# Kernel tuning notes

Hardware: AMD Instinct MI355X
Metric: run time of the kernel (lower is better)

## Reference

```python
import jax, jax.numpy as jnp
import numpy as np

SEQ, B, I, H = 512, 64, 1024, 1024

def setup_inputs() -> dict:
    key = jax.random.key(0)
    ks = jax.random.split(key, 6)
    scale_ih = 1.0 / np.sqrt(I)
    scale_hh = 1.0 / np.sqrt(H)
    return {
        "input": jax.random.normal(ks[0], (SEQ, B, I), dtype=jnp.float32),
        "h_0": jax.random.normal(ks[1], (1, B, H), dtype=jnp.float32),
        "weight_ih": jax.random.normal(ks[2], (3 * H, I), dtype=jnp.float32) * scale_ih,
        "weight_hh": jax.random.normal(ks[3], (3 * H, H), dtype=jnp.float32) * scale_hh,
        "bias_ih": jax.random.normal(ks[4], (3 * H,), dtype=jnp.float32) * scale_hh,
        "bias_hh": jax.random.normal(ks[5], (3 * H,), dtype=jnp.float32) * scale_hh,
    }


def _gru_lbr0(input, h0, weight_ih, weight_hh, bias_ih, bias_hh):
    """Unidirectional GRU, ONNX linear_before_reset=0 semantics.

    r_t = sigmoid(x W_ir^T + b_ir + h W_hr^T + b_hr)
    z_t = sigmoid(x W_iz^T + b_iz + h W_hz^T + b_hz)
    n_t = tanh(x W_in^T + b_in + (r_t * h) W_hn^T + b_hn)
    h_t = (1 - z_t) * n_t + z_t * h
    """
    hidden = h0.shape[-1]
    # Precompute all input projections in one big GEMM: (S, B, 3H)
    gx = jnp.einsum('sbi,gi->sbg', input, weight_ih) + bias_ih
    W_hr, W_hz, W_hn = jnp.split(weight_hh, 3, axis=0)
    b_hr, b_hz, b_hn = jnp.split(bias_hh, 3, axis=0)

    def step(h, gx_t):
        gx_r, gx_z, gx_n = jnp.split(gx_t, 3, axis=-1)
        r = jax.nn.sigmoid(gx_r + h @ W_hr.T + b_hr)
        z = jax.nn.sigmoid(gx_z + h @ W_hz.T + b_hz)
        n = jnp.tanh(gx_n + (r * h) @ W_hn.T + b_hn)
        h_new = (1.0 - z) * n + z * h
        return h_new, h_new

    h_n, outputs = jax.lax.scan(step, h0, gx)
    return outputs, h_n  # (S, B, H), (B, H)


def reference(input, h_0, weight_ih, weight_hh, bias_ih, bias_hh):
    seq_len, batch, _ = input.shape
    hidden = weight_hh.shape[1]
    outputs, h_n = _gru_lbr0(input, h_0[0], weight_ih, weight_hh, bias_ih, bias_hh)
    # Match GRUWrapper output layout: Y = (S, num_dir=1, B, H), Y_h = (1, B, H)
    Y = outputs.reshape(seq_len, batch, 1, hidden).transpose(0, 2, 1, 3)
    Y_h = h_n[None, :, :]
    return (Y, Y_h)
```

## Files before the change

kernel.cpp:

```cpp
#include <hip/hip_runtime.h>

typedef unsigned short ushort_t;
typedef short sh8 __attribute__((ext_vector_type(8)));
typedef float f32x4 __attribute__((ext_vector_type(4)));

#define MFMA16(a,b,c) __builtin_amdgcn_mfma_f32_16x16x32_bf16((a),(b),(c),0,0,0)

#define SEQL   512
#define BATCH  64
#define HDIM   1024
#define G3     3072
#define AROWS  (SEQL*BATCH)
#define YSZ    (SEQL*BATCH*HDIM)
#define BH     (BATCH*HDIM)
#define NWG    64

__device__ __forceinline__ ushort_t f2bf(float x) {
  unsigned u = __float_as_uint(x);
  u += 0x7FFFu + ((u >> 16) & 1u);
  return (ushort_t)(u >> 16);
}
__device__ __forceinline__ float bf2f(ushort_t h) {
  return __uint_as_float(((unsigned)h) << 16);
}

__global__ void cvt_kernel(const float* __restrict__ wih, const float* __restrict__ h0,
                           ushort_t* __restrict__ WihH, ushort_t* __restrict__ WihL,
                           ushort_t* __restrict__ hH) {
  const int NW = G3 * HDIM;
  int i0 = blockIdx.x * blockDim.x + threadIdx.x;
  int stride = gridDim.x * blockDim.x;
  for (int i = i0; i < NW; i += stride) {
    float x = wih[i]; ushort_t h = f2bf(x);
    WihH[i] = h; WihL[i] = f2bf(x - bf2f(h));
  }
  for (int i = i0; i < BH; i += stride) {
    hH[i] = f2bf(h0[i]);
  }
}

__global__ __launch_bounds__(256) void gemm_gx(
    const float* __restrict__ A,
    const ushort_t* __restrict__ BHp, const ushort_t* __restrict__ BLp,
    const float* __restrict__ bias,
    float* __restrict__ gx)
{
  int bid = blockIdx.x;
  int mt = bid / 24, nt = bid % 24;
  int w = threadIdx.x >> 6, l = threadIdx.x & 63;
  int lr = l & 15, lk = (l >> 4) * 8;

  f32x4 acc[2][8];
  #pragma unroll
  for (int mi = 0; mi < 2; ++mi)
    #pragma unroll
    for (int ni = 0; ni < 8; ++ni) acc[mi][ni] = (f32x4){0.f, 0.f, 0.f, 0.f};

  int arow0 = mt * 128 + w * 32 + lr;
  int brow0 = nt * 128 + lr;

  for (int k0 = 0; k0 < HDIM; k0 += 32) {
    int ka = k0 + lk;
    sh8 aH[2];
    #pragma unroll
    for (int mi = 0; mi < 2; ++mi) {
      const float* ap = A + (size_t)(arow0 + mi * 16) * HDIM + ka;
      float4 x0 = *(const float4*)ap;
      float4 x1 = *(const float4*)(ap + 4);
      float xs[8] = {x0.x, x0.y, x0.z, x0.w, x1.x, x1.y, x1.z, x1.w};
      #pragma unroll
      for (int j = 0; j < 8; ++j) aH[mi][j] = (short)f2bf(xs[j]);
    }
    #pragma unroll
    for (int ni = 0; ni < 8; ++ni) {
      const ushort_t* bh = BHp + (size_t)(brow0 + ni * 16) * HDIM + ka;
      const ushort_t* bl = BLp + (size_t)(brow0 + ni * 16) * HDIM + ka;
      sh8 bHf = *(const sh8*)bh;
      sh8 bLf = *(const sh8*)bl;
      #pragma unroll
      for (int mi = 0; mi < 2; ++mi) {
        acc[mi][ni] = MFMA16(aH[mi], bHf, acc[mi][ni]);
        acc[mi][ni] = MFMA16(aH[mi], bLf, acc[mi][ni]);
      }
    }
  }
  int rb = (l >> 4) * 4;
  #pragma unroll
  for (int mi = 0; mi < 2; ++mi)
    #pragma unroll
    for (int ni = 0; ni < 8; ++ni) {
      int col = nt * 128 + ni * 16 + lr;
      float b = bias[col];
      #pragma unroll
      for (int j = 0; j < 4; ++j) {
        int row = mt * 128 + w * 32 + mi * 16 + rb + j;
        __builtin_nontemporal_store(acc[mi][ni][j] + b, &gx[(size_t)row * G3 + col]);
      }
    }
}

__device__ __forceinline__ void gbar_flat(unsigned* slots, int g, int tid, unsigned e) {
  __syncthreads();
  if (tid < 64) {
    if (tid == 0)
      __hip_atomic_store(slots + g * 32, e, __ATOMIC_RELEASE, __HIP_MEMORY_SCOPE_AGENT);
    unsigned* sp = slots + tid * 32;
    while (__hip_atomic_load(sp, __ATOMIC_RELAXED, __HIP_MEMORY_SCOPE_AGENT) < e)
      __builtin_amdgcn_s_sleep(1);
    (void)__hip_atomic_load(sp, __ATOMIC_ACQUIRE, __HIP_MEMORY_SCOPE_AGENT);
  }
  __syncthreads();
}

__global__ __launch_bounds__(256, 1) void gru_rec(
    const float* __restrict__ gx,
    const float* __restrict__ whh,
    const float* __restrict__ bhh,
    const float* __restrict__ h0f,
    ushort_t* __restrict__ hH,
    ushort_t* __restrict__ rhH,
    float* __restrict__ Y, float* __restrict__ Yh,
    unsigned* __restrict__ slots)
{
  extern __shared__ char lds[];
  const int g = blockIdx.x;
  const int tid = threadIdx.x;
  const int w = tid >> 6, l = tid & 63;
  const int lr = l & 15, lk = (l >> 4) * 8, rb = (l >> 4) * 4;
  const int c0 = g * 16, m0 = w * 16;
  const int c = c0 + lr;

  #pragma unroll
  for (int p = 0; p < 32; ++p) {
    int q = tid + p * 256;
    int flat = q * 16;
    int lrow = flat >> 11;
    int off = flat & 2047;
    int dst = flat ^ ((lrow & 7) << 4);
    int col = off >> 1;
    const float* src;
    bool lo = false;
    if (lrow < 16)      src = whh + (size_t)(c0 + lrow) * HDIM + col;
    else if (lrow < 32) src = whh + (size_t)(1024 + c0 + lrow - 16) * HDIM + col;
    else if (lrow < 48) src = whh + (size_t)(2048 + c0 + lrow - 32) * HDIM + col;
    else              { src = whh + (size_t)(2048 + c0 + lrow - 48) * HDIM + col; lo = true; }
    float4 x0 = *(const float4*)src;
    float4 x1 = *(const float4*)(src + 4);
    float xs[8] = {x0.x, x0.y, x0.z, x0.w, x1.x, x1.y, x1.z, x1.w};
    union { ushort_t v[8]; sh8 s; } pk;
    #pragma unroll
    for (int j = 0; j < 8; ++j) {
      ushort_t hi = f2bf(xs[j]);
      pk.v[j] = lo ? f2bf(xs[j] - bf2f(hi)) : hi;
    }
    *(sh8*)(lds + dst) = pk.s;
  }
  __syncthreads();

  const float br = bhh[c], bz = bhh[1024 + c], bn = bhh[2048 + c];
  unsigned bar = 0;

  float hold[4];
  #pragma unroll
  for (int j = 0; j < 4; ++j) hold[j] = h0f[(m0 + rb + j) * HDIM + c];

  float gxr[4], gxz[4], gxn[4];
  #pragma unroll
  for (int j = 0; j < 4; ++j) {
    int b = m0 + rb + j;
    gxr[j] = __builtin_nontemporal_load(gx + (size_t)b * G3 + c);
    gxz[j] = __builtin_nontemporal_load(gx + (size_t)b * G3 + 1024 + c);
    gxn[j] = __builtin_nontemporal_load(gx + (size_t)b * G3 + 2048 + c);
  }

  for (int t = 0; t < SEQL; ++t) {
    const int par = t & 1;

    const ushort_t* ha = hH + par * BH + (size_t)(m0 + lr) * HDIM + lk;
    sh8 bufa[32];
    #pragma unroll
    for (int i = 0; i < 32; ++i) bufa[i] = *(const sh8*)(ha + i * 32);

    f32x4 accR = (f32x4){0,0,0,0}, accZ = (f32x4){0,0,0,0};
    #pragma unroll
    for (int i = 0; i < 32; ++i) {
      int byt = ((lr << 11) + ((i * 32 + lk) << 1)) ^ ((lr & 7) << 4);
      sh8 rW = *(const sh8*)(lds + byt);
      sh8 zW = *(const sh8*)(lds + 32768 + byt);
      accR = MFMA16(bufa[i], rW, accR);
      accZ = MFMA16(bufa[i], zW, accZ);
    }

    float zreg[4];
    #pragma unroll
    for (int j = 0; j < 4; ++j) {
      int b = m0 + rb + j;
      float pr = accR[j] + gxr[j] + br;
      float pz = accZ[j] + gxz[j] + bz;
      float r = 1.f / (1.f + __expf(-pr));
      zreg[j] = 1.f / (1.f + __expf(-pz));
      rhH[b * HDIM + c] = f2bf(r * hold[j]);
    }
    ++bar;
    gbar_flat(slots, g, tid, bar);

    const ushort_t* ra = rhH + (size_t)(m0 + lr) * HDIM + lk;
    #pragma unroll
    for (int i = 0; i < 32; ++i) bufa[i] = *(const sh8*)(ra + i * 32);

    int tn = (t + 1 < SEQL) ? t + 1 : t;
    {
      const float* gxn2 = gx + (size_t)tn * (BATCH * G3);
      #pragma unroll
      for (int j = 0; j < 4; ++j) {
        int b = m0 + rb + j;
        gxr[j] = __builtin_nontemporal_load(gxn2 + (size_t)b * G3 + c);
        gxz[j] = __builtin_nontemporal_load(gxn2 + (size_t)b * G3 + 1024 + c);
      }
    }

    f32x4 accN = (f32x4){0,0,0,0};
    #pragma unroll
    for (int i = 0; i < 32; ++i) {
      int byt = ((lr << 11) + ((i * 32 + lk) << 1)) ^ ((lr & 7) << 4);
      sh8 nW = *(const sh8*)(lds + 65536 + byt);
      sh8 nLo = *(const sh8*)(lds + 98304 + byt);
      accN = MFMA16(bufa[i], nW, accN);
      accN = MFMA16(bufa[i], nLo, accN);
    }

    ushort_t* hHn = hH + (par ^ 1) * BH;
    float gxnN[4];
    {
      const float* gxn2 = gx + (size_t)tn * (BATCH * G3);
      #pragma unroll
      for (int j = 0; j < 4; ++j) {
        int b = m0 + rb + j;
        gxnN[j] = __builtin_nontemporal_load(gxn2 + (size_t)b * G3 + 2048 + c);
      }
    }
    #pragma unroll
    for (int j = 0; j < 4; ++j) {
      int b = m0 + rb + j;
      float pn = accN[j] + gxn[j] + bn;
      float n = tanhf(pn);
      float z = zreg[j];
      float hnew = (1.f - z) * n + z * hold[j];
      hold[j] = hnew;
      __builtin_nontemporal_store(hnew, &Y[(size_t)t * BH + b * HDIM + c]);
      hHn[b * HDIM + c] = f2bf(hnew);
      if (t == SEQL - 1) __builtin_nontemporal_store(hnew, &Yh[b * HDIM + c]);
    }
    #pragma unroll
    for (int j = 0; j < 4; ++j) gxn[j] = gxnN[j];

    if (t < SEQL - 1) {
      ++bar;
      gbar_flat(slots, g, tid, bar);
    }
  }
}

extern "C" void kernel_launch(void* const* d_in, const int* in_sizes, int n_in,
                              void* d_out, int out_size, void* d_ws, size_t ws_size,
                              hipStream_t stream) {
  const float* input = (const float*)d_in[0];
  const float* h0    = (const float*)d_in[1];
  const float* wih   = (const float*)d_in[2];
  const float* whh   = (const float*)d_in[3];
  const float* bih   = (const float*)d_in[4];
  const float* bhh   = (const float*)d_in[5];

  char* ws = (char*)d_ws;
  size_t o = 0;
  float* gx = (float*)(ws + o);         o += (size_t)AROWS * G3 * 4;
  ushort_t* WihH = (ushort_t*)(ws + o); o += (size_t)G3 * HDIM * 2;
  ushort_t* WihL = (ushort_t*)(ws + o); o += (size_t)G3 * HDIM * 2;
  ushort_t* hH = (ushort_t*)(ws + o);   o += 2 * (size_t)BH * 2;
  ushort_t* rhH = (ushort_t*)(ws + o);  o += (size_t)BH * 2;
  unsigned* slots = (unsigned*)(ws + o); o += (size_t)NWG * 128;

  float* Y  = (float*)d_out;
  float* Yh = (float*)d_out + (size_t)YSZ;

  (void)hipFuncSetAttribute((const void*)gru_rec,
                            hipFuncAttributeMaxDynamicSharedMemorySize, 131072);

  (void)hipMemsetAsync(slots, 0, (size_t)NWG * 128, stream);
  cvt_kernel<<<2048, 256, 0, stream>>>(wih, h0, WihH, WihL, hH);
  gemm_gx<<<(AROWS / 128) * (G3 / 128), 256, 0, stream>>>(input, WihH, WihL, bih, gx);
  gru_rec<<<64, 256, 131072, stream>>>(gx, whh, bhh, h0, hH, rhH, Y, Yh, slots);
}
```

Measured before the change: 8.889 ms.

## Split recurrent GRU across batch groups with split-K waves and per-group barriers

Launches 256 workgroups arranged as 4 independent batch groups of 64, each synchronising only within its group. Inside a workgroup the four waves split the hidden-dimension reduction and combine partial MFMA accumulators through LDS, and wave 0 applies the gate math. This cuts per-step MFMA and load latency per workgroup and shrinks barrier scope. In exchange it adds LDS reductions and extra block syncs, replicates weight staging, and requires all 256 persistent workgroups to be co-resident.

```diff
diff --git a/kernel.cpp b/kernel.cpp
--- a/kernel.cpp
+++ b/kernel.cpp
@@ -13,7 +13,7 @@
 #define AROWS  (SEQL*BATCH)
 #define YSZ    (SEQL*BATCH*HDIM)
 #define BH     (BATCH*HDIM)
-#define NWG    64
+#define NWGR   256
 
 __device__ __forceinline__ ushort_t f2bf(float x) {
   unsigned u = __float_as_uint(x);
@@ -99,12 +99,13 @@
     }
 }
 
-__device__ __forceinline__ void gbar_flat(unsigned* slots, int g, int tid, unsigned e) {
+__device__ __forceinline__ void gbar_grp(unsigned* slots, int q, int jj, int tid, unsigned e) {
   __syncthreads();
   if (tid < 64) {
+    unsigned* base = slots + (size_t)q * 64 * 32;
     if (tid == 0)
-      __hip_atomic_store(slots + g * 32, e, __ATOMIC_RELEASE, __HIP_MEMORY_SCOPE_AGENT);
-    unsigned* sp = slots + tid * 32;
+      __hip_atomic_store(base + jj * 32, e, __ATOMIC_RELEASE, __HIP_MEMORY_SCOPE_AGENT);
+    unsigned* sp = base + tid * 32;
     while (__hip_atomic_load(sp, __ATOMIC_RELAXED, __HIP_MEMORY_SCOPE_AGENT) < e)
       __builtin_amdgcn_s_sleep(1);
     (void)__hip_atomic_load(sp, __ATOMIC_ACQUIRE, __HIP_MEMORY_SCOPE_AGENT);
@@ -124,16 +125,19 @@
 {
   extern __shared__ char lds[];
   const int g = blockIdx.x;
+  const int q = g >> 6;
+  const int jj = g & 63;
   const int tid = threadIdx.x;
   const int w = tid >> 6, l = tid & 63;
   const int lr = l & 15, lk = (l >> 4) * 8, rb = (l >> 4) * 4;
-  const int c0 = g * 16, m0 = w * 16;
+  const int c0 = jj * 16;
   const int c = c0 + lr;
+  const int b0 = q * 16;
 
   #pragma unroll
   for (int p = 0; p < 32; ++p) {
-    int q = tid + p * 256;
-    int flat = q * 16;
+    int qq = tid + p * 256;
+    int flat = qq * 16;
     int lrow = flat >> 11;
     int off = flat & 2047;
     int dst = flat ^ ((lrow & 7) << 4);
@@ -155,108 +159,102 @@
     }
     *(sh8*)(lds + dst) = pk.s;
   }
+  f32x4* sR = (f32x4*)(lds + 131072);
+  f32x4* sZ = (f32x4*)(lds + 131072 + 4096);
   __syncthreads();
 
   const float br = bhh[c], bz = bhh[1024 + c], bn = bhh[2048 + c];
   unsigned bar = 0;
 
-  float hold[4];
-  #pragma unroll
-  for (int j = 0; j < 4; ++j) hold[j] = h0f[(m0 + rb + j) * HDIM + c];
-
-  float gxr[4], gxz[4], gxn[4];
-  #pragma unroll
-  for (int j = 0; j < 4; ++j) {
-    int b = m0 + rb + j;
-    gxr[j] = __builtin_nontemporal_load(gx + (size_t)b * G3 + c);
-    gxz[j] = __builtin_nontemporal_load(gx + (size_t)b * G3 + 1024 + c);
-    gxn[j] = __builtin_nontemporal_load(gx + (size_t)b * G3 + 2048 + c);
+  float hold[4], zreg[4], gxr[4], gxz[4], gxn[4];
+  if (w == 0) {
+    #pragma unroll
+    for (int j = 0; j < 4; ++j) {
+      int b = b0 + rb + j;
+      hold[j] = h0f[b * HDIM + c];
+      gxr[j] = __builtin_nontemporal_load(gx + (size_t)b * G3 + c);
+      gxz[j] = __builtin_nontemporal_load(gx + (size_t)b * G3 + 1024 + c);
+      gxn[j] = __builtin_nontemporal_load(gx + (size_t)b * G3 + 2048 + c);
+    }
   }
 
   for (int t = 0; t < SEQL; ++t) {
     const int par = t & 1;
 
-    const ushort_t* ha = hH + par * BH + (size_t)(m0 + lr) * HDIM + lk;
-    sh8 bufa[32];
-    #pragma unroll
-    for (int i = 0; i < 32; ++i) bufa[i] = *(const sh8*)(ha + i * 32);
+    const ushort_t* ha = hH + par * BH + (size_t)(b0 + lr) * HDIM + 256 * w + lk;
+    sh8 bufa[8];
+    #pragma unroll
+    for (int i = 0; i < 8; ++i) bufa[i] = *(const sh8*)(ha + i * 32);
 
     f32x4 accR = (f32x4){0,0,0,0}, accZ = (f32x4){0,0,0,0};
     #pragma unroll
-    for (int i = 0; i < 32; ++i) {
-      int byt = ((lr << 11) + ((i * 32 + lk) << 1)) ^ ((lr & 7) << 4);
+    for (int i = 0; i < 8; ++i) {
+      int kk = 8 * w + i;
+      int byt = ((lr << 11) + ((kk * 32 + lk) << 1)) ^ ((lr & 7) << 4);
       sh8 rW = *(const sh8*)(lds + byt);
       sh8 zW = *(const sh8*)(lds + 32768 + byt);
       accR = MFMA16(bufa[i], rW, accR);
       accZ = MFMA16(bufa[i], zW, accZ);
     }
-
-    float zreg[4];
-    #pragma unroll
-    for (int j = 0; j < 4; ++j) {
-      int b = m0 + rb + j;
-      float pr = accR[j] + gxr[j] + br;
-      float pz = accZ[j] + gxz[j] + bz;
-      float r = 1.f / (1.f + __expf(-pr));
-      zreg[j] = 1.f / (1.f + __expf(-pz));
-      rhH[b * HDIM + c] = f2bf(r * hold[j]);
+    sR[w * 64 + l] = accR;
+    sZ[w * 64 + l] = accZ;
+    __syncthreads();
+    if (w == 0) {
+      accR = sR[l] + sR[64 + l] + sR[128 + l] + sR[192 + l];
+      accZ = sZ[l] + sZ[64 + l] + sZ[128 + l] + sZ[192 + l];
+      #pragma unroll
+      for (int j = 0; j < 4; ++j) {
+        int b = b0 + rb + j;
+        float pr = accR[j] + gxr[j] + br;
+        float pz = accZ[j] + gxz[j] + bz;
+        float r = 1.f / (1.f + __expf(-pr));
+        zreg[j] = 1.f / (1.f + __expf(-pz));
+        rhH[b * HDIM + c] = f2bf(r * hold[j]);
+      }
     }
     ++bar;
-    gbar_flat(slots, g, tid, bar);
-
-    const ushort_t* ra = rhH + (size_t)(m0 + lr) * HDIM + lk;
-    #pragma unroll
-    for (int i = 0; i < 32; ++i) bufa[i] = *(const sh8*)(ra + i * 32);
-
-    int tn = (t + 1 < SEQL) ? t + 1 : t;
-    {
-      const float* gxn2 = gx + (size_t)tn * (BATCH * G3);
-      #pragma unroll
-      for (int j = 0; j < 4; ++j) {
-        int b = m0 + rb + j;
-        gxr[j] = __builtin_nontemporal_load(gxn2 + (size_t)b * G3 + c);
-        gxz[j] = __builtin_nontemporal_load(gxn2 + (size_t)b * G3 + 1024 + c);
-      }
-    }
+    gbar_grp(slots, q, jj, tid, bar);
+
+    const ushort_t* ra = rhH + (size_t)(b0 + lr) * HDIM + 256 * w + lk;
+    #pragma unroll
+    for (int i = 0; i < 8; ++i) bufa[i] = *(const sh8*)(ra + i * 32);
 
     f32x4 accN = (f32x4){0,0,0,0};
     #pragma unroll
-    for (int i = 0; i < 32; ++i) {
-      int byt = ((lr << 11) + ((i * 32 + lk) << 1)) ^ ((lr & 7) << 4);
+    for (int i = 0; i < 8; ++i) {
+      int kk = 8 * w + i;
+      int byt = ((lr << 11) + ((kk * 32 + lk) << 1)) ^ ((lr & 7) << 4);
       sh8 nW = *(const sh8*)(lds + 65536 + byt);
       sh8 nLo = *(const sh8*)(lds + 98304 + byt);
       accN = MFMA16(bufa[i], nW, accN);
       accN = MFMA16(bufa[i], nLo, accN);
     }
-
-    ushort_t* hHn = hH + (par ^ 1) * BH;
-    float gxnN[4];
-    {
-      const float* gxn2 = gx + (size_t)tn * (BATCH * G3);
+    sR[w * 64 + l] = accN;
+    __syncthreads();
+    if (w == 0) {
+      accN = sR[l] + sR[64 + l] + sR[128 + l] + sR[192 + l];
+      int tn = (t + 1 < SEQL) ? t + 1 : t;
+      const float* gxt1 = gx + (size_t)tn * (BATCH * G3);
+      ushort_t* hHn = hH + (par ^ 1) * BH;
       #pragma unroll
       for (int j = 0; j < 4; ++j) {
-        int b = m0 + rb + j;
-        gxnN[j] = __builtin_nontemporal_load(gxn2 + (size_t)b * G3 + 2048 + c);
-      }
-    }
-    #pragma unroll
-    for (int j = 0; j < 4; ++j) {
-      int b = m0 + rb + j;
-      float pn = accN[j] + gxn[j] + bn;
-      float n = tanhf(pn);
-      float z = zreg[j];
-      float hnew = (1.f - z) * n + z * hold[j];
-      hold[j] = hnew;
-      __builtin_nontemporal_store(hnew, &Y[(size_t)t * BH + b * HDIM + c]);
-      hHn[b * HDIM + c] = f2bf(hnew);
-      if (t == SEQL - 1) __builtin_nontemporal_store(hnew, &Yh[b * HDIM + c]);
-    }
-    #pragma unroll
-    for (int j = 0; j < 4; ++j) gxn[j] = gxnN[j];
-
+        int b = b0 + rb + j;
+        float pn = accN[j] + gxn[j] + bn;
+        float n = tanhf(pn);
+        float z = zreg[j];
+        float hnew = (1.f - z) * n + z * hold[j];
+        hold[j] = hnew;
+        __builtin_nontemporal_store(hnew, &Y[(size_t)t * BH + b * HDIM + c]);
+        hHn[b * HDIM + c] = f2bf(hnew);
+        if (t == SEQL - 1) __builtin_nontemporal_store(hnew, &Yh[b * HDIM + c]);
+        gxr[j] = __builtin_nontemporal_load(gxt1 + (size_t)b * G3 + c);
+        gxz[j] = __builtin_nontemporal_load(gxt1 + (size_t)b * G3 + 1024 + c);
+        gxn[j] = __builtin_nontemporal_load(gxt1 + (size_t)b * G3 + 2048 + c);
+      }
+    }
     if (t < SEQL - 1) {
       ++bar;
-      gbar_flat(slots, g, tid, bar);
+      gbar_grp(slots, q, jj, tid, bar);
     }
   }
 }
@@ -278,16 +276,16 @@
   ushort_t* WihL = (ushort_t*)(ws + o); o += (size_t)G3 * HDIM * 2;
   ushort_t* hH = (ushort_t*)(ws + o);   o += 2 * (size_t)BH * 2;
   ushort_t* rhH = (ushort_t*)(ws + o);  o += (size_t)BH * 2;
-  unsigned* slots = (unsigned*)(ws + o); o += (size_t)NWG * 128;
+  unsigned* slots = (unsigned*)(ws + o); o += (size_t)NWGR * 128;
 
   float* Y  = (float*)d_out;
   float* Yh = (float*)d_out + (size_t)YSZ;
 
   (void)hipFuncSetAttribute((const void*)gru_rec,
-                            hipFuncAttributeMaxDynamicSharedMemorySize, 131072);
-
-  (void)hipMemsetAsync(slots, 0, (size_t)NWG * 128, stream);
+                            hipFuncAttributeMaxDynamicSharedMemorySize, 139264);
+
+  (void)hipMemsetAsync(slots, 0, (size_t)NWGR * 128, stream);
   cvt_kernel<<<2048, 256, 0, stream>>>(wih, h0, WihH, WihL, hH);
   gemm_gx<<<(AROWS / 128) * (G3 / 128), 256, 0, stream>>>(input, WihH, WihL, bih, gx);
-  gru_rec<<<64, 256, 131072, stream>>>(gx, whh, bhh, h0, hH, rhH, Y, Yh, slots);
-}
+  gru_rec<<<NWGR, 256, 139264, stream>>>(gx, whh, bhh, h0, hH, rhH, Y, Yh, slots);
+}
```

Measured after the change: 16.87 ms. +89.8%, slower.
